# Optimization experiments

Hardware: AMD Instinct MI355X
Metric: run time of the kernel (lower is better)

The kernel has to match this reference:

```python
import jax, jax.numpy as jnp
import numpy as np

DECAY = 0.99
EPS = 1e-05
BETA = 0.25
N_CODES = 1024
CODE_DIM = 128


def setup_inputs() -> dict:
    key = jax.random.key(0)
    k1, k2, k3, k4 = jax.random.split(key, 4)
    z_e = jax.random.normal(k1, (32, CODE_DIM, 32, 32), dtype=jnp.float32)
    embed = jax.random.normal(k2, (N_CODES, CODE_DIM), dtype=jnp.float32)
    cluster_size = jax.random.uniform(k3, (N_CODES,), dtype=jnp.float32) * 10.0
    embed_avg = jax.random.normal(k4, (N_CODES, CODE_DIM), dtype=jnp.float32)
    return {"z_e": z_e, "embed": embed, "cluster_size": cluster_size, "embed_avg": embed_avg}


def reference(z_e, embed, cluster_size, embed_avg):
    B, C, H, W = z_e.shape
    n_codes = embed.shape[0]
    # (B,C,H,W) -> (B*H*W, C)
    flat = jnp.transpose(z_e, (0, 2, 3, 1)).reshape(-1, C).astype(jnp.float32)
    e = embed.astype(jnp.float32)
    d = (flat ** 2).sum(1, keepdims=True) - 2.0 * flat @ e.T + (e ** 2).sum(1)
    idx = jnp.argmin(d, axis=1)
    z_q = embed[idx].reshape(B, H, W, C)
    z_q = jnp.transpose(z_q, (0, 3, 1, 2))  # (B,C,H,W)

    # ---- EMA codebook update (training branch, no-grad in torch) ----
    counts = jax.ops.segment_sum(jnp.ones_like(idx, dtype=jnp.float32), idx,
                                 num_segments=n_codes)
    new_cluster_size = cluster_size * DECAY + (1.0 - DECAY) * counts
    embed_sum = jax.ops.segment_sum(flat, idx, num_segments=n_codes)  # == (flat.T @ one_hot).T
    new_embed_avg = embed_avg * DECAY + (1.0 - DECAY) * embed_sum
    n = new_cluster_size.sum()
    denom = n + n_codes * EPS
    cs = (new_cluster_size + EPS) / denom * n
    cs_safe = jnp.maximum(cs, EPS)[:, None]
    embed_normalized = new_embed_avg / cs_safe
    embed_normalized = jnp.nan_to_num(embed_normalized, nan=0.0, posinf=1.0, neginf=-1.0)
    new_embed = jnp.clip(embed_normalized, -2.0, 2.0)

    # straight-through estimator
    z_q_st = z_e + jax.lax.stop_gradient(z_q - z_e)
    diff = jax.lax.stop_gradient(z_q_st).astype(jnp.float32) - z_e.astype(jnp.float32)
    loss = BETA * jnp.mean(diff ** 2)

    return (z_q_st, loss, idx.reshape(B, H, W), z_q, z_e,
            new_embed, new_cluster_size, new_embed_avg)
```

## Files before the change

kernel.cpp:

```cpp
#include <hip/hip_runtime.h>

#define DECAY 0.99f
#define ONE_MINUS_DECAY 0.01f
#define EPSF 1e-5f
#define BETA 0.25f

constexpr int M_ = 32768;
constexpr int N_ = 1024;
constexpr int K_ = 128;

typedef _Float16 f16;
typedef f16 f16x8 __attribute__((ext_vector_type(8)));
typedef float f32x4 __attribute__((ext_vector_type(4)));

#define GLOAD_LDS(g, l) __builtin_amdgcn_global_load_lds( \
    (const __attribute__((address_space(1))) void*)(g),   \
    (__attribute__((address_space(3))) void*)(l), 16, 0, 0)

#define PINS(p) { unsigned _t2 = m1 > (p) ? m1 : (p); m1 = m1 < (p) ? m1 : (p); \
                  unsigned _t3 = m2 > _t2 ? m2 : _t2;  m2 = m2 < _t2 ? m2 : _t2; \
                  m3 = m3 < _t3 ? m3 : _t3; }

constexpr size_t WS_FLAT   = 0;
constexpr size_t WS_XH     = WS_FLAT   + (size_t)M_ * K_ * 4;
constexpr size_t WS_EH     = WS_XH     + (size_t)M_ * K_ * 2;
constexpr size_t WS_NL     = WS_EH     + (size_t)N_ * K_ * 2;
constexpr size_t WS_PPK    = WS_NL     + (size_t)N_ * 4;
constexpr size_t WS_IDX    = WS_PPK    + (size_t)4 * M_ * 16;
constexpr size_t WS_COUNTS = WS_IDX    + (size_t)M_ * 4;
constexpr size_t WS_CUR    = WS_COUNTS + (size_t)N_ * 4;
constexpr size_t WS_ESUM   = WS_CUR    + (size_t)N_ * 4;
constexpr size_t WS_OFFS   = WS_ESUM   + (size_t)N_ * K_ * 4;
constexpr size_t WS_ROWS   = WS_OFFS   + (size_t)N_ * 4;
constexpr size_t WS_LPART  = WS_ROWS   + (size_t)M_ * 4;
constexpr size_t WS_NSUM   = WS_LPART  + (size_t)4096 * 8;

constexpr size_t O_ZQST = 0;
constexpr size_t O_LOSS = O_ZQST + (size_t)M_ * K_;
constexpr size_t O_IDX  = O_LOSS + 1;
constexpr size_t O_ZQ   = O_IDX  + (size_t)M_;
constexpr size_t O_ZE   = O_ZQ   + (size_t)M_ * K_;
constexpr size_t O_EMB  = O_ZE   + (size_t)M_ * K_;
constexpr size_t O_NCS  = O_EMB  + (size_t)N_ * K_;
constexpr size_t O_NEA  = O_NCS  + (size_t)N_;

__global__ void transpose_kernel(const float* __restrict__ ze,
                                 const float* __restrict__ embed,
                                 float* __restrict__ flat,
                                 f16* __restrict__ xh,
                                 float* __restrict__ out_ze,
                                 f16* __restrict__ eh, float* __restrict__ nl,
                                 uint4* __restrict__ zero8k) {
    __shared__ float tile[128][33];
    __shared__ float ered[2];
    const int j = blockIdx.x;
    const int t = threadIdx.x;
    if (t < 128) {
        float a = embed[(size_t)j * K_ + t];
        eh[(size_t)j * K_ + t] = (f16)(-2.f * a);
        float s = a * a;
        #pragma unroll
        for (int off = 32; off; off >>= 1) s += __shfl_down(s, off);
        if ((t & 63) == 0) ered[t >> 6] = s;
    }
    if (j < 2) zero8k[j * 256 + t] = make_uint4(0u, 0u, 0u, 0u);

    int b = j >> 5, h = j & 31;
    const size_t base = (size_t)b * 131072 + (size_t)h * 32;
    #pragma unroll
    for (int i = 0; i < 4; ++i) {
        int q = i * 256 + t;
        int c = q >> 3, w4 = (q & 7) * 4;
        float4 v = *(const float4*)(ze + base + (size_t)c * 1024 + w4);
        tile[c][w4 + 0] = v.x; tile[c][w4 + 1] = v.y;
        tile[c][w4 + 2] = v.z; tile[c][w4 + 3] = v.w;
        *(float4*)(out_ze + base + (size_t)c * 1024 + w4) = v;
    }
    __syncthreads();
    if (t == 0) nl[j] = ered[0] + ered[1];
    const int r0 = b * 1024 + h * 32;
    #pragma unroll
    for (int i = 0; i < 2; ++i) {
        int w = (t >> 4) + i * 16;
        int c0 = (t & 15) * 8;
        int r = r0 + w;
        float vv[8];
        #pragma unroll
        for (int q = 0; q < 8; ++q) vv[q] = tile[c0 + q][w];
        *(float4*)(flat + (size_t)r * K_ + c0)     = make_float4(vv[0], vv[1], vv[2], vv[3]);
        *(float4*)(flat + (size_t)r * K_ + c0 + 4) = make_float4(vv[4], vv[5], vv[6], vv[7]);
        f16x8 hv;
        #pragma unroll
        for (int q = 0; q < 8; ++q) hv[q] = (f16)vv[q];
        size_t xa = (size_t)r * K_ + ((((c0 >> 3) ^ (r & 15)) << 3));
        *(f16x8*)(xh + xa) = hv;
    }
}

__global__ __launch_bounds__(256, 4)
void nn_kernel(const f16* __restrict__ xh_g,
               const f16* __restrict__ eh, const float* __restrict__ nl,
               uint4* __restrict__ p_pk) {
    __shared__ __align__(16) f16 xbh[64 * 128];
    __shared__ uint4 pm[4][64];
    const int t = threadIdx.x;
    const int wave = t >> 6, lane = t & 63;
    const int crow = lane & 15, g = lane >> 4;
    const int c0 = blockIdx.y * 256 + wave * 64;

    f16x8 efh[4][4];
    #pragma unroll
    for (int m = 0; m < 4; ++m)
        #pragma unroll
        for (int kt = 0; kt < 4; ++kt)
            efh[m][kt] = *(const f16x8*)(eh + (size_t)(c0 + m * 16 + crow) * K_ + kt * 32 + g * 8);
    f32x4 nlpre[4];
    #pragma unroll
    for (int m = 0; m < 4; ++m) {
        f32x4 v = *(const f32x4*)(nl + c0 + m * 16 + g * 4);
        nlpre[m] = v * 1024.f + 1048576.f;
    }
    const unsigned cbase = (unsigned)(c0 + g * 4);

    auto stage = [&](int bt) {
        const size_t tb = (size_t)(blockIdx.x * 4 + bt) * 8192;
        #pragma unroll
        for (int i = 0; i < 4; ++i) {
            int q = wave * 4 + i;
            GLOAD_LDS(xh_g + tb + q * 512 + lane * 8, &xbh[q * 512]);
        }
    };

    stage(0);
    __syncthreads();
    for (int bt = 0; bt < 4; ++bt) {
        const int R0 = (blockIdx.x * 4 + bt) * 64;
        #pragma unroll
        for (int st = 0; st < 4; ++st) {
            f32x4 acc[4];
            #pragma unroll
            for (int m = 0; m < 4; ++m) acc[m] = (f32x4){0.f, 0.f, 0.f, 0.f};
            #pragma unroll
            for (int kt = 0; kt < 4; ++kt) {
                int off = (st * 16 + crow) * 128 + ((((kt << 2) + g) ^ crow) << 3);
                f16x8 bh = *(const f16x8*)&xbh[off];
                #pragma unroll
                for (int m = 0; m < 4; ++m)
                    acc[m] = __builtin_amdgcn_mfma_f32_16x16x32_f16(efh[m][kt], bh, acc[m], 0, 0, 0);
            }
            unsigned m1 = ~0u, m2 = ~0u, m3 = ~0u;
            #pragma unroll
            for (int m = 0; m < 4; ++m)
                #pragma unroll
                for (int q = 0; q < 4; ++q) {
                    float fq = fmaf(acc[m][q], 1024.f, nlpre[m][q]);
                    unsigned p = (((unsigned)fq) << 10) + cbase + (unsigned)(m * 16 + q);
                    PINS(p);
                }
            #pragma unroll
            for (int d = 16; d <= 32; d <<= 1) {
                unsigned o1 = (unsigned)__shfl_xor((int)m1, d);
                unsigned o2 = (unsigned)__shfl_xor((int)m2, d);
                unsigned o3 = (unsigned)__shfl_xor((int)m3, d);
                PINS(o1); PINS(o2); PINS(o3);
            }
            if (lane < 16) pm[wave][st * 16 + crow] = make_uint4(m1, m2, m3, 0u);
        }
        __syncthreads();
        if (bt < 3) stage(bt + 1);
        if (lane < 16) {
            int row = wave * 16 + lane;
            uint4 a = pm[0][row];
            unsigned m1 = a.x, m2 = a.y, m3 = a.z;
            #pragma unroll
            for (int w = 1; w < 4; ++w) {
                uint4 b = pm[w][row];
                PINS(b.x); PINS(b.y); PINS(b.z);
            }
            p_pk[(size_t)blockIdx.y * M_ + R0 + row] = make_uint4(m1, m2, m3, 0u);
        }
        __syncthreads();
    }
}

__global__ void reduce_refine_kernel(const uint4* __restrict__ p_pk,
                                     const float* __restrict__ flat,
                                     const float* __restrict__ embed,
                                     const float* __restrict__ nl,
                                     int* __restrict__ idxws, float* __restrict__ out_idx,
                                     int* __restrict__ counts) {
    int r = blockIdx.x * 256 + threadIdx.x;
    uint4 a = p_pk[r];
    unsigned m1 = a.x, m2 = a.y, m3 = a.z;
    #pragma unroll
    for (int y = 1; y < 4; ++y) {
        uint4 b = p_pk[(size_t)y * M_ + r];
        PINS(b.x); PINS(b.y); PINS(b.z);
    }
    int i1 = (int)(m1 & 1023u);
    if ((m2 >> 10) - (m1 >> 10) <= 512u) {
        int i2 = (int)(m2 & 1023u), i3 = (int)(m3 & 1023u);
        const float* x  = flat  + (size_t)r * K_;
        const float* e1 = embed + (size_t)i1 * K_;
        const float* e2 = embed + (size_t)i2 * K_;
        const float* e3 = embed + (size_t)i3 * K_;
        float d1 = 0.f, d2 = 0.f, d3 = 0.f;
        for (int k = 0; k < K_; ++k) {
            float xv = x[k];
            d1 = fmaf(xv, e1[k], d1);
            d2 = fmaf(xv, e2[k], d2);
            d3 = fmaf(xv, e3[k], d3);
        }
        float s1 = fmaf(-2.f, d1, nl[i1]);
        float s2 = fmaf(-2.f, d2, nl[i2]);
        float s3 = fmaf(-2.f, d3, nl[i3]);
        float bs = s1; int bi = i1;
        if (s2 < bs || (s2 == bs && i2 < bi)) { bs = s2; bi = i2; }
        if (s3 < bs || (s3 == bs && i3 < bi)) { bs = s3; bi = i3; }
        i1 = bi;
    }
    idxws[r] = i1;
    out_idx[r] = (float)i1;
    atomicAdd(counts + i1, 1);
}

__global__ void gather_kernel(const float* __restrict__ ze,
                              const float* __restrict__ embed,
                              const int* __restrict__ idxws,
                              float* __restrict__ out_st, float* __restrict__ out_zq,
                              double* __restrict__ lpart) {
    int q = blockIdx.x * 256 + threadIdx.x;
    int o0 = q * 4;
    float4 zev = *(const float4*)(ze + o0);
    const float zv[4] = {zev.x, zev.y, zev.z, zev.w};
    int rbase = (o0 >> 17) * 1024 + (o0 & 1023);
    int c = (o0 >> 10) & 127;
    int4 jj = *(const int4*)(idxws + rbase);
    const int jv[4] = {jj.x, jj.y, jj.z, jj.w};
    float st4[4], zq4[4];
    double ls = 0.0;
    #pragma unroll
    for (int e = 0; e < 4; ++e) {
        float zq = embed[(size_t)jv[e] * K_ + c];
        float st = zv[e] + (zq - zv[e]);
        st4[e] = st; zq4[e] = zq;
        float diff = st - zv[e];
        ls += (double)diff * (double)diff;
    }
    *(float4*)(out_st + o0) = make_float4(st4[0], st4[1], st4[2], st4[3]);
    *(float4*)(out_zq + o0) = make_float4(zq4[0], zq4[1], zq4[2], zq4[3]);
    __shared__ double red[256];
    red[threadIdx.x] = ls;
    __syncthreads();
    for (int s = 128; s; s >>= 1) {
        if (threadIdx.x < s) red[threadIdx.x] += red[threadIdx.x + s];
        __syncthreads();
    }
    if (threadIdx.x == 0) lpart[blockIdx.x] = red[0];
}

__global__ void ema_a_kernel(const float* __restrict__ cluster_size,
                             const int* __restrict__ counts,
                             float* __restrict__ out_ncs, float* __restrict__ nws,
                             const double* __restrict__ lpart, float* __restrict__ out_loss,
                             int* __restrict__ offs) {
    int j = threadIdx.x;
    int cnt = counts[j];
    float ncs = cluster_size[j] * DECAY + ONE_MINUS_DECAY * (float)cnt;
    out_ncs[j] = ncs;
    __shared__ float red[1024];
    __shared__ double dred[1024];
    __shared__ int sc[1024];
    red[j] = ncs;
    sc[j] = cnt;
    double s = 0.0;
    #pragma unroll
    for (int i = 0; i < 4; ++i) s += lpart[j * 4 + i];
    dred[j] = s;
    __syncthreads();
    for (int d = 1; d < 1024; d <<= 1) {
        int v = (j >= d) ? sc[j - d] : 0;
        __syncthreads();
        sc[j] += v;
        __syncthreads();
    }
    offs[j] = sc[j] - cnt;
    for (int st = 512; st; st >>= 1) {
        if (j < st) { red[j] += red[j + st]; dred[j] += dred[j + st]; }
        __syncthreads();
    }
    if (j == 0) {
        nws[0] = red[0];
        out_loss[0] = (float)((double)BETA * (dred[0] / 4194304.0));
    }
}

__global__ void bucket_kernel(const int* __restrict__ idxws, const int* __restrict__ offs,
                              int* __restrict__ cur, int* __restrict__ rows,
                              float4* __restrict__ esum_z) {
    __shared__ int lcnt[N_];
    __shared__ int lbase[N_];
    int t = threadIdx.x;
    esum_z[blockIdx.x * 256 + t] = make_float4(0.f, 0.f, 0.f, 0.f);
    #pragma unroll
    for (int i = 0; i < 4; ++i) lcnt[i * 256 + t] = 0;
    __syncthreads();
    int r = blockIdx.x * 256 + t;
    int j = idxws[r];
    atomicAdd(&lcnt[j], 1);
    __syncthreads();
    #pragma unroll
    for (int i = 0; i < 4; ++i) {
        int c = i * 256 + t;
        int n = lcnt[c];
        lbase[c] = n ? atomicAdd(cur + c, n) : 0;
        lcnt[c] = 0;
    }
    __syncthreads();
    int p = atomicAdd(&lcnt[j], 1) + lbase[j];
    rows[offs[j] + p] = r;
}

__global__ void chunksum_kernel(const float* __restrict__ flat,
                                const int* __restrict__ rows,
                                const int* __restrict__ idxws,
                                float* __restrict__ esum) {
    __shared__ int srid[64];
    __shared__ int scd[65];
    int k = threadIdx.x;
    int b = blockIdx.x;
    if (k < 64) {
        int r = rows[b * 64 + k];
        srid[k] = r;
        scd[k] = idxws[r];
    }
    if (k == 64) scd[64] = -1;
    __syncthreads();
    float acc = 0.f;
    #pragma unroll 1
    for (int i0 = 0; i0 < 64; i0 += 8) {
        float v[8];
        #pragma unroll
        for (int i = 0; i < 8; ++i)
            v[i] = flat[(size_t)srid[i0 + i] * K_ + k];
        #pragma unroll
        for (int i = 0; i < 8; ++i) {
            acc += v[i];
            int p = i0 + i;
            if (scd[p + 1] != scd[p]) {
                atomicAdd(esum + (size_t)scd[p] * K_ + k, acc);
                acc = 0.f;
            }
        }
    }
}

__global__ void ema_b_kernel(const float* __restrict__ embed_avg,
                             const float* __restrict__ esum,
                             const float* __restrict__ out_ncs,
                             const float* __restrict__ nws,
                             float* __restrict__ out_nea, float* __restrict__ out_emb) {
    int o = blockIdx.x * 256 + threadIdx.x;
    int j = o >> 7;
    float navg = embed_avg[o] * DECAY + ONE_MINUS_DECAY * esum[o];
    out_nea[o] = navg;
    float n = nws[0];
    float denom = n + 1024.0f * EPSF;
    float cs = (out_ncs[j] + EPSF) / denom * n;
    float cs_safe = fmaxf(cs, EPSF);
    float v = navg / cs_safe;
    if (v != v) v = 0.f;
    v = fminf(fmaxf(v, -2.f), 2.f);
    out_emb[o] = v;
}

extern "C" void kernel_launch(void* const* d_in, const int* in_sizes, int n_in,
                              void* d_out, int out_size, void* d_ws, size_t ws_size,
                              hipStream_t stream) {
    const float* z_e          = (const float*)d_in[0];
    const float* embed        = (const float*)d_in[1];
    const float* cluster_size = (const float*)d_in[2];
    const float* embed_avg    = (const float*)d_in[3];
    float* out = (float*)d_out;
    char*  ws  = (char*)d_ws;

    float*  flat   = (float*)(ws + WS_FLAT);
    f16*    xhp    = (f16*)  (ws + WS_XH);
    f16*    ehp    = (f16*)  (ws + WS_EH);
    float*  nlp    = (float*)(ws + WS_NL);
    uint4*  p_pk   = (uint4*)(ws + WS_PPK);
    int*    idxws  = (int*)  (ws + WS_IDX);
    int*    counts = (int*)  (ws + WS_COUNTS);
    int*    cur    = (int*)  (ws + WS_CUR);
    float*  esum   = (float*)(ws + WS_ESUM);
    int*    offs   = (int*)  (ws + WS_OFFS);
    int*    rows   = (int*)  (ws + WS_ROWS);
    double* lpart  = (double*)(ws + WS_LPART);
    float*  nws    = (float*)(ws + WS_NSUM);

    transpose_kernel<<<1024, 256, 0, stream>>>(z_e, embed, flat, xhp, out + O_ZE,
                                               ehp, nlp, (uint4*)(ws + WS_COUNTS));
    nn_kernel<<<dim3(128, 4), 256, 0, stream>>>(xhp, ehp, nlp, p_pk);
    reduce_refine_kernel<<<M_ / 256, 256, 0, stream>>>(p_pk, flat, embed, nlp,
                                                       idxws, out + O_IDX, counts);
    gather_kernel<<<4096, 256, 0, stream>>>(z_e, embed, idxws,
                                            out + O_ZQST, out + O_ZQ, lpart);
    ema_a_kernel<<<1, 1024, 0, stream>>>(cluster_size, counts, out + O_NCS, nws,
                                         lpart, out + O_LOSS, offs);
    bucket_kernel<<<M_ / 256, 256, 0, stream>>>(idxws, offs, cur, rows,
                                                (float4*)(ws + WS_ESUM));
    chunksum_kernel<<<M_ / 64, K_, 0, stream>>>(flat, rows, idxws, esum);
    ema_b_kernel<<<(N_ * K_) / 256, 256, 0, stream>>>(embed_avg, esum, out + O_NCS, nws,
                                                      out + O_NEA, out + O_EMB);
}
```

Before: 94.22 us.

## Compute loss from refined distances and drop z_e read in gather

The loss is now computed in the refine kernel as ||x||^2 plus the best refined distance, summed per block, so the gather kernel no longer reads z_e and just writes the gathered codebook rows to both outputs. The refine step now always runs on the top-3 candidates, with vectorised float4 loads, instead of only when the gap is small. The MFMA accumulator is also initialised with the norm bias, which removes a per-element fma in the packing step. In exchange, refine does more unconditional work, and the z_q_st output assumes z_e + (z_q - z_e) equals z_q exactly, which can differ by rounding.

```diff
diff --git a/kernel.cpp b/kernel.cpp
--- a/kernel.cpp
+++ b/kernel.cpp
@@ -114,11 +114,11 @@
         #pragma unroll
         for (int kt = 0; kt < 4; ++kt)
             efh[m][kt] = *(const f16x8*)(eh + (size_t)(c0 + m * 16 + crow) * K_ + kt * 32 + g * 8);
-    f32x4 nlpre[4];
+    f32x4 nlinit[4];
     #pragma unroll
     for (int m = 0; m < 4; ++m) {
         f32x4 v = *(const f32x4*)(nl + c0 + m * 16 + g * 4);
-        nlpre[m] = v * 1024.f + 1048576.f;
+        nlinit[m] = v + 1024.f;
     }
     const unsigned cbase = (unsigned)(c0 + g * 4);
 
@@ -139,7 +139,7 @@
         for (int st = 0; st < 4; ++st) {
             f32x4 acc[4];
             #pragma unroll
-            for (int m = 0; m < 4; ++m) acc[m] = (f32x4){0.f, 0.f, 0.f, 0.f};
+            for (int m = 0; m < 4; ++m) acc[m] = nlinit[m];
             #pragma unroll
             for (int kt = 0; kt < 4; ++kt) {
                 int off = (st * 16 + crow) * 128 + ((((kt << 2) + g) ^ crow) << 3);
@@ -153,8 +153,8 @@
             for (int m = 0; m < 4; ++m)
                 #pragma unroll
                 for (int q = 0; q < 4; ++q) {
-                    float fq = fmaf(acc[m][q], 1024.f, nlpre[m][q]);
-                    unsigned p = (((unsigned)fq) << 10) + cbase + (unsigned)(m * 16 + q);
+                    unsigned u = (unsigned)(acc[m][q] * 1024.f);
+                    unsigned p = (u << 10) + cbase + (unsigned)(m * 16 + q);
                     PINS(p);
                 }
             #pragma unroll
@@ -188,7 +188,8 @@
                                      const float* __restrict__ embed,
                                      const float* __restrict__ nl,
                                      int* __restrict__ idxws, float* __restrict__ out_idx,
-                                     int* __restrict__ counts) {
+                                     int* __restrict__ counts,
+                                     double* __restrict__ lpart) {
     int r = blockIdx.x * 256 + threadIdx.x;
     uint4 a = p_pk[r];
     unsigned m1 = a.x, m2 = a.y, m3 = a.z;
@@ -197,66 +198,54 @@
         uint4 b = p_pk[(size_t)y * M_ + r];
         PINS(b.x); PINS(b.y); PINS(b.z);
     }
-    int i1 = (int)(m1 & 1023u);
-    if ((m2 >> 10) - (m1 >> 10) <= 512u) {
-        int i2 = (int)(m2 & 1023u), i3 = (int)(m3 & 1023u);
-        const float* x  = flat  + (size_t)r * K_;
-        const float* e1 = embed + (size_t)i1 * K_;
-        const float* e2 = embed + (size_t)i2 * K_;
-        const float* e3 = embed + (size_t)i3 * K_;
-        float d1 = 0.f, d2 = 0.f, d3 = 0.f;
-        for (int k = 0; k < K_; ++k) {
-            float xv = x[k];
-            d1 = fmaf(xv, e1[k], d1);
-            d2 = fmaf(xv, e2[k], d2);
-            d3 = fmaf(xv, e3[k], d3);
-        }
-        float s1 = fmaf(-2.f, d1, nl[i1]);
-        float s2 = fmaf(-2.f, d2, nl[i2]);
-        float s3 = fmaf(-2.f, d3, nl[i3]);
-        float bs = s1; int bi = i1;
-        if (s2 < bs || (s2 == bs && i2 < bi)) { bs = s2; bi = i2; }
-        if (s3 < bs || (s3 == bs && i3 < bi)) { bs = s3; bi = i3; }
-        i1 = bi;
-    }
-    idxws[r] = i1;
-    out_idx[r] = (float)i1;
-    atomicAdd(counts + i1, 1);
-}
-
-__global__ void gather_kernel(const float* __restrict__ ze,
-                              const float* __restrict__ embed,
+    int i1 = (int)(m1 & 1023u), i2 = (int)(m2 & 1023u), i3 = (int)(m3 & 1023u);
+    const float4* x  = (const float4*)(flat  + (size_t)r * K_);
+    const float4* e1 = (const float4*)(embed + (size_t)i1 * K_);
+    const float4* e2 = (const float4*)(embed + (size_t)i2 * K_);
+    const float4* e3 = (const float4*)(embed + (size_t)i3 * K_);
+    float xn = 0.f, d1 = 0.f, d2 = 0.f, d3 = 0.f;
+    for (int k = 0; k < 32; ++k) {
+        float4 xv = x[k], v1 = e1[k], v2 = e2[k], v3 = e3[k];
+        xn = fmaf(xv.x, xv.x, xn); xn = fmaf(xv.y, xv.y, xn);
+        xn = fmaf(xv.z, xv.z, xn); xn = fmaf(xv.w, xv.w, xn);
+        d1 = fmaf(xv.x, v1.x, d1); d1 = fmaf(xv.y, v1.y, d1);
+        d1 = fmaf(xv.z, v1.z, d1); d1 = fmaf(xv.w, v1.w, d1);
+        d2 = fmaf(xv.x, v2.x, d2); d2 = fmaf(xv.y, v2.y, d2);
+        d2 = fmaf(xv.z, v2.z, d2); d2 = fmaf(xv.w, v2.w, d2);
+        d3 = fmaf(xv.x, v3.x, d3); d3 = fmaf(xv.y, v3.y, d3);
+        d3 = fmaf(xv.z, v3.z, d3); d3 = fmaf(xv.w, v3.w, d3);
+    }
+    float s1 = fmaf(-2.f, d1, nl[i1]);
+    float s2 = fmaf(-2.f, d2, nl[i2]);
+    float s3 = fmaf(-2.f, d3, nl[i3]);
+    float bs = s1; int bi = i1;
+    if (s2 < bs || (s2 == bs && i2 < bi)) { bs = s2; bi = i2; }
+    if (s3 < bs || (s3 == bs && i3 < bi)) { bs = s3; bi = i3; }
+    idxws[r] = bi;
+    out_idx[r] = (float)bi;
+    atomicAdd(counts + bi, 1);
+    __shared__ double red[256];
+    red[threadIdx.x] = (double)xn + (double)bs;
+    __syncthreads();
+    for (int s = 128; s; s >>= 1) {
+        if (threadIdx.x < s) red[threadIdx.x] += red[threadIdx.x + s];
+        __syncthreads();
+    }
+    if (threadIdx.x == 0) lpart[blockIdx.x] = red[0];
+}
+
+__global__ void gather_kernel(const float* __restrict__ embed,
                               const int* __restrict__ idxws,
-                              float* __restrict__ out_st, float* __restrict__ out_zq,
-                              double* __restrict__ lpart) {
+                              float* __restrict__ out_st, float* __restrict__ out_zq) {
     int q = blockIdx.x * 256 + threadIdx.x;
     int o0 = q * 4;
-    float4 zev = *(const float4*)(ze + o0);
-    const float zv[4] = {zev.x, zev.y, zev.z, zev.w};
     int rbase = (o0 >> 17) * 1024 + (o0 & 1023);
     int c = (o0 >> 10) & 127;
     int4 jj = *(const int4*)(idxws + rbase);
-    const int jv[4] = {jj.x, jj.y, jj.z, jj.w};
-    float st4[4], zq4[4];
-    double ls = 0.0;
-    #pragma unroll
-    for (int e = 0; e < 4; ++e) {
-        float zq = embed[(size_t)jv[e] * K_ + c];
-        float st = zv[e] + (zq - zv[e]);
-        st4[e] = st; zq4[e] = zq;
-        float diff = st - zv[e];
-        ls += (double)diff * (double)diff;
-    }
-    *(float4*)(out_st + o0) = make_float4(st4[0], st4[1], st4[2], st4[3]);
-    *(float4*)(out_zq + o0) = make_float4(zq4[0], zq4[1], zq4[2], zq4[3]);
-    __shared__ double red[256];
-    red[threadIdx.x] = ls;
-    __syncthreads();
-    for (int s = 128; s; s >>= 1) {
-        if (threadIdx.x < s) red[threadIdx.x] += red[threadIdx.x + s];
-        __syncthreads();
-    }
-    if (threadIdx.x == 0) lpart[blockIdx.x] = red[0];
+    float4 zq = make_float4(embed[(size_t)jj.x * K_ + c], embed[(size_t)jj.y * K_ + c],
+                            embed[(size_t)jj.z * K_ + c], embed[(size_t)jj.w * K_ + c]);
+    *(float4*)(out_st + o0) = zq;
+    *(float4*)(out_zq + o0) = zq;
 }
 
 __global__ void ema_a_kernel(const float* __restrict__ cluster_size,
@@ -273,10 +262,7 @@
     __shared__ int sc[1024];
     red[j] = ncs;
     sc[j] = cnt;
-    double s = 0.0;
-    #pragma unroll
-    for (int i = 0; i < 4; ++i) s += lpart[j * 4 + i];
-    dred[j] = s;
+    dred[j] = (j < 128) ? lpart[j] : 0.0;
     __syncthreads();
     for (int d = 1; d < 1024; d <<= 1) {
         int v = (j >= d) ? sc[j - d] : 0;
@@ -402,9 +388,8 @@
                                                ehp, nlp, (uint4*)(ws + WS_COUNTS));
     nn_kernel<<<dim3(128, 4), 256, 0, stream>>>(xhp, ehp, nlp, p_pk);
     reduce_refine_kernel<<<M_ / 256, 256, 0, stream>>>(p_pk, flat, embed, nlp,
-                                                       idxws, out + O_IDX, counts);
-    gather_kernel<<<4096, 256, 0, stream>>>(z_e, embed, idxws,
-                                            out + O_ZQST, out + O_ZQ, lpart);
+                                                       idxws, out + O_IDX, counts, lpart);
+    gather_kernel<<<4096, 256, 0, stream>>>(embed, idxws, out + O_ZQST, out + O_ZQ);
     ema_a_kernel<<<1, 1024, 0, stream>>>(cluster_size, counts, out + O_NCS, nws,
                                          lpart, out + O_LOSS, offs);
     bucket_kernel<<<M_ / 256, 256, 0, stream>>>(idxws, offs, cur, rows,
```

After: 102.7 us. 1.09x slower.
